# Optimization experiments

Measured on AMD Instinct MI355X. Metric: run time of the kernel, lower is better.

The kernel has to match this reference:

```python
import jax, jax.numpy as jnp
import numpy as np

B, L, S, D, H, CTX = 2, 2048, 512, 1024, 16, 1024
HD = D // H
HID = 4 * D
EPS = 1e-6


def _ln(x):
    mu = jnp.mean(x, axis=-1, keepdims=True)
    var = jnp.mean((x - mu) ** 2, axis=-1, keepdims=True)
    return (x - mu) * jax.lax.rsqrt(var + EPS)


def _rotate_half(x):
    x1, x2 = jnp.split(x, 2, axis=-1)
    return jnp.concatenate([-x2, x1], axis=-1)


def _heads(t):  # [B,N,D] -> [B,H,N,HD]
    return t.reshape(t.shape[0], t.shape[1], H, HD).transpose(0, 2, 1, 3)


def _merge(t):  # [B,H,N,HD] -> [B,N,D]
    return t.transpose(0, 2, 1, 3).reshape(t.shape[0], t.shape[2], D)


def setup_inputs() -> dict:
    key = jax.random.key(0)
    ks = jax.random.split(key, 24)
    s = 0.02
    inp = {
        "x": jax.random.normal(ks[0], (B, L, D), jnp.float32),
        "timestep_emb": jax.random.normal(ks[1], (B, D), jnp.float32),
        "context_emb": jax.random.normal(ks[2], (B, S, CTX), jnp.float32),
        "rope_emb": jax.random.normal(ks[3], (L, HD), jnp.float32),
        # adaLN modulation: Linear(D -> 6D) with bias
        "w_mod": jax.random.normal(ks[4], (D, 6 * D), jnp.float32) * s,
        "b_mod": jnp.zeros((6 * D,), jnp.float32),
        # self-attention (no qkv bias, out has bias)
        "wq_s": jax.random.normal(ks[5], (D, D), jnp.float32) * s,
        "wk_s": jax.random.normal(ks[6], (D, D), jnp.float32) * s,
        "wv_s": jax.random.normal(ks[7], (D, D), jnp.float32) * s,
        "wo_s": jax.random.normal(ks[8], (D, D), jnp.float32) * s,
        "bo_s": jnp.zeros((D,), jnp.float32),
        # cross-attention (q/k/v no bias, out has bias)
        "wq_c": jax.random.normal(ks[9], (D, D), jnp.float32) * s,
        "wk_c": jax.random.normal(ks[10], (CTX, D), jnp.float32) * s,
        "wv_c": jax.random.normal(ks[11], (CTX, D), jnp.float32) * s,
        "wo_c": jax.random.normal(ks[12], (D, D), jnp.float32) * s,
        "bo_c": jnp.zeros((D,), jnp.float32),
        # MLP
        "w1": jax.random.normal(ks[13], (D, HID), jnp.float32) * s,
        "b1": jnp.zeros((HID,), jnp.float32),
        "w2": jax.random.normal(ks[14], (HID, D), jnp.float32) * s,
        "b2": jnp.zeros((D,), jnp.float32),
    }
    return inp


def reference(x, timestep_emb, context_emb, rope_emb,
              w_mod, b_mod,
              wq_s, wk_s, wv_s, wo_s, bo_s,
              wq_c, wk_c, wv_c, wo_c, bo_c,
              w1, b1, w2, b2):
    scale = HD ** -0.5
    # adaLN modulation from timestep embedding
    mods = jnp.split(timestep_emb @ w_mod + b_mod, 6, axis=-1)
    shift_msa, scale_msa, gate_msa, shift_mlp, scale_mlp, gate_mlp = mods

    # --- self-attention with RoPE ---
    nx = _ln(x) * (1.0 + scale_msa[:, None, :]) + shift_msa[:, None, :]
    q = _heads(nx @ wq_s)
    k = _heads(nx @ wk_s)
    v = _heads(nx @ wv_s)
    cos = jnp.cos(rope_emb)[None, None]  # [1,1,L,HD]
    sin = jnp.sin(rope_emb)[None, None]
    q = q * cos + _rotate_half(q) * sin
    k = k * cos + _rotate_half(k) * sin
    attn = jax.nn.softmax(jnp.einsum("bhqd,bhkd->bhqk", q, k) * scale, axis=-1)
    sa = _merge(jnp.einsum("bhqk,bhkd->bhqd", attn, v)) @ wo_s + bo_s
    x = x + gate_msa[:, None, :] * sa

    # --- cross-attention (no mask) ---
    nx = _ln(x)
    q = _heads(nx @ wq_c)
    k = _heads(context_emb @ wk_c)
    v = _heads(context_emb @ wv_c)
    attn = jax.nn.softmax(jnp.einsum("bhqd,bhkd->bhqk", q, k) * scale, axis=-1)
    ca = _merge(jnp.einsum("bhqk,bhkd->bhqd", attn, v)) @ wo_c + bo_c
    x = x + ca

    # --- MLP with modulation + gate ---
    nx = _ln(x) * (1.0 + scale_mlp[:, None, :]) + shift_mlp[:, None, :]
    h = jax.nn.gelu(nx @ w1 + b1, approximate=False)
    x = x + gate_mlp[:, None, :] * (h @ w2 + b2)
    return x
```

## Files before the change

### kernel.cpp

```cpp
#include <hip/hip_runtime.h>
#include <hip/hip_bf16.h>


typedef short short8 __attribute__((ext_vector_type(8)));
typedef float f32x4 __attribute__((ext_vector_type(4)));
typedef float f32x16 __attribute__((ext_vector_type(16)));

#define DEV __device__ __forceinline__

DEV unsigned short f2b(float f) {
  __hip_bfloat16 h = __float2bfloat16(f);
  return *reinterpret_cast<unsigned short*>(&h);
}
DEV float b2f(unsigned short u) {
  unsigned int x = ((unsigned int)u) << 16;
  return __builtin_bit_cast(float, x);
}
DEV unsigned int pk2(float lo, float hi) {
  return (unsigned int)f2b(lo) | ((unsigned int)f2b(hi) << 16);
}
DEV void vpsw(unsigned int& a, unsigned int& b) {
  asm("v_permlane32_swap_b32 %0, %1" : "+v"(a), "+v"(b));
}

#define GLB(p) ((const __attribute__((address_space(1))) void*)(p))
#define LDSP(p) ((__attribute__((address_space(3))) void*)(p))

__global__ __launch_bounds__(256) void transpose_cast(
    const float* __restrict__ in, unsigned short* __restrict__ out, int R, int C) {
  __shared__ float tile[32][33];
  int bx = blockIdx.x * 32, by = blockIdx.y * 32;
  int tx = threadIdx.x, ty = threadIdx.y;
#pragma unroll
  for (int i = ty; i < 32; i += 8)
    tile[i][tx] = in[(size_t)(by + i) * C + bx + tx];
  __syncthreads();
#pragma unroll
  for (int i = ty; i < 32; i += 8)
    out[(size_t)(bx + i) * R + by + tx] = f2b(tile[tx][i]);
}

__global__ __launch_bounds__(256) void cast_bf16(
    const float* __restrict__ in, unsigned short* __restrict__ out, int n) {
  int i = blockIdx.x * 256 + threadIdx.x;
  if (i < n) out[i] = f2b(in[i]);
}

__global__ __launch_bounds__(256) void rope_tab(
    const float* __restrict__ rope, float* __restrict__ cosT, float* __restrict__ sinT, int n) {
  int i = blockIdx.x * 256 + threadIdx.x;
  if (i < n) {
    float v = rope[i];
    cosT[i] = cosf(v);
    sinT[i] = sinf(v);
  }
}

__global__ __launch_bounds__(256) void mods_kernel(
    const float* __restrict__ te, const unsigned short* __restrict__ wmodT,
    const float* __restrict__ bmod, float* __restrict__ mods) {
  int w = blockIdx.x * 4 + (threadIdx.x >> 6);
  int lane = threadIdx.x & 63;
  int b = w / 6144, j = w % 6144;
  const unsigned short* wr = wmodT + (size_t)j * 1024;
  const float* ter = te + (size_t)b * 1024;
  int k0 = lane * 16;
  float sum = 0.f;
#pragma unroll
  for (int u = 0; u < 2; ++u) {
    short8 wv = *(const short8*)(wr + k0 + u * 8);
#pragma unroll
    for (int e = 0; e < 8; ++e)
      sum += b2f((unsigned short)wv[e]) * ter[k0 + u * 8 + e];
  }
#pragma unroll
  for (int off = 32; off >= 1; off >>= 1) sum += __shfl_down(sum, off);
  if (lane == 0) mods[(size_t)b * 6144 + j] = sum + bmod[j];
}

__global__ __launch_bounds__(256) void ln_mod(
    const float* __restrict__ x, const float* __restrict__ mods,
    unsigned short* __restrict__ out, int scale_ofs, int shift_ofs) {
  int row = blockIdx.x;
  int b = row >> 11;
  int tid = threadIdx.x;
  const float* xr = x + (size_t)row * 1024;
  float4 v = ((const float4*)xr)[tid];
  float s = v.x + v.y + v.z + v.w;
  float ss = v.x * v.x + v.y * v.y + v.z * v.z + v.w * v.w;
#pragma unroll
  for (int off = 32; off >= 1; off >>= 1) {
    s += __shfl_down(s, off);
    ss += __shfl_down(ss, off);
  }
  __shared__ float red[8];
  int wave = tid >> 6, lane = tid & 63;
  if (lane == 0) { red[wave] = s; red[4 + wave] = ss; }
  __syncthreads();
  if (tid == 0) {
    float S = red[0] + red[1] + red[2] + red[3];
    float SS = red[4] + red[5] + red[6] + red[7];
    float mu = S * (1.f / 1024.f);
    red[0] = mu;
    red[1] = SS * (1.f / 1024.f) - mu * mu;
  }
  __syncthreads();
  float mu = red[0];
  float rs = rsqrtf(red[1] + 1e-6f);
  float vv[4] = {v.x, v.y, v.z, v.w};
  unsigned short o[4];
#pragma unroll
  for (int c = 0; c < 4; ++c) {
    int col = tid * 4 + c;
    float nv = (vv[c] - mu) * rs;
    if (scale_ofs >= 0)
      nv = nv * (1.f + mods[(size_t)b * 6144 + scale_ofs + col]) +
           mods[(size_t)b * 6144 + shift_ofs + col];
    o[c] = f2b(nv);
  }
  *(ushort4*)(&out[(size_t)row * 1024 + tid * 4]) = *(const ushort4*)o;
}

__global__ __launch_bounds__(256) void rope_apply(
    unsigned short* __restrict__ qb, unsigned short* __restrict__ kb,
    const float* __restrict__ cosT, const float* __restrict__ sinT) {
  int idx = blockIdx.x * 256 + threadIdx.x;
  unsigned short* buf = blockIdx.y ? kb : qb;
  int row = idx >> 9;
  int rem = idx & 511;
  int h = rem >> 5, d = rem & 31;
  int l = row & 2047;
  size_t base = (size_t)row * 1024 + h * 64 + d;
  float x1 = b2f(buf[base]), x2 = b2f(buf[base + 32]);
  float c1 = cosT[l * 64 + d], s1 = sinT[l * 64 + d];
  float c2 = cosT[l * 64 + d + 32], s2 = sinT[l * 64 + d + 32];
  buf[base] = f2b(x1 * c1 - x2 * s1);
  buf[base + 32] = f2b(x2 * c2 + x1 * s2);
}

template <int EPI, int MI, int NJ>
DEV void gemm_epilogue(f32x4 (&acc)[MI][NJ], void* Cout, const float* bias,
                       const float* mods, int gate_ofs, const float* src,
                       int N, int rowsPerB, int m0, int n0, int wm, int wn,
                       int g, int r) {
#pragma unroll
  for (int i = 0; i < MI; ++i) {
#pragma unroll
    for (int j = 0; j < NJ; ++j) {
#pragma unroll
      for (int q = 0; q < 4; ++q) {
        size_t grow = (size_t)(m0 + wm + i * 16 + g * 4 + q);
        size_t gcol = (size_t)(n0 + wn + j * 16 + r);
        float v = acc[i][j][q];
        if constexpr (EPI == 0) {
          ((unsigned short*)Cout)[grow * N + gcol] = f2b(v);
        } else if constexpr (EPI == 1) {
          v += bias[gcol];
          float ge = 0.5f * v * (1.0f + erff(v * 0.70710678f));
          ((unsigned short*)Cout)[grow * N + gcol] = f2b(ge);
        } else if constexpr (EPI == 3) {
          size_t buf = gcol >> 10;
          ((unsigned short*)Cout)[buf * (4096ull * 1024) + grow * 1024 + (gcol & 1023)] = f2b(v);
        } else {
          v += bias[gcol];
          float gate = 1.0f;
          if (gate_ofs >= 0)
            gate = mods[(grow / rowsPerB) * 6144 + gate_ofs + gcol];
          ((float*)Cout)[grow * N + gcol] = src[grow * N + gcol] + gate * v;
        }
      }
    }
  }
}

template <int EPI>
__global__ __launch_bounds__(256, 2) void gemm_bt(
    const unsigned short* __restrict__ A, const unsigned short* __restrict__ Bt,
    void* __restrict__ Cout, const float* __restrict__ bias,
    const float* __restrict__ mods, int gate_ofs, const float* __restrict__ src,
    int M, int N, int K, int rowsPerB) {
  __shared__ unsigned short As[128 * 32];
  __shared__ unsigned short Bs[128 * 32];
  const int tid = threadIdx.x;
  const int wave = tid >> 6, lane = tid & 63;
  const int g = lane >> 4, r = lane & 15;
  const int m0 = blockIdx.y * 128, n0 = blockIdx.x * 128;
  const int wm = (wave >> 1) * 64, wn = (wave & 1) * 64;
  const int srow = lane >> 2;
  const int scol = (lane & 3) * 8;

  f32x4 acc[4][4] = {};

  for (int k0 = 0; k0 < K; k0 += 32) {
    __syncthreads();
#pragma unroll
    for (int cc = 0; cc < 4; ++cc) {
      int c = wave * 4 + cc;
      int isB = c >> 3;
      int cl = c & 7;
      int row = cl * 16 + srow;
      const unsigned short* gsrc =
          isB ? (Bt + (size_t)(n0 + row) * K + k0 + scol)
              : (A + (size_t)(m0 + row) * K + k0 + scol);
      unsigned short* ldst = (isB ? Bs : As) + cl * 512;
      __builtin_amdgcn_global_load_lds(GLB(gsrc), LDSP(ldst), 16, 0, 0);
    }
    __syncthreads();

    short8 bfr[4];
#pragma unroll
    for (int j = 0; j < 4; ++j)
      bfr[j] = *(const short8*)(&Bs[(wn + j * 16 + r) * 32 + g * 8]);
#pragma unroll
    for (int i = 0; i < 4; ++i) {
      short8 af = *(const short8*)(&As[(wm + i * 16 + r) * 32 + g * 8]);
#pragma unroll
      for (int j = 0; j < 4; ++j)
        acc[i][j] = __builtin_amdgcn_mfma_f32_16x16x32_bf16(af, bfr[j], acc[i][j], 0, 0, 0);
    }
  }
  gemm_epilogue<EPI, 4, 4>(acc, Cout, bias, mods, gate_ofs, src, N, rowsPerB,
                           m0, n0, wm, wn, g, r);
}

template <int EPI>
__global__ __launch_bounds__(256) void gemm_pipe(
    const unsigned short* __restrict__ A, const unsigned short* __restrict__ Bt,
    void* __restrict__ Cout, const float* __restrict__ bias,
    const float* __restrict__ mods, int gate_ofs, const float* __restrict__ src,
    int M, int N, int K, int rowsPerB, int mshift) {
  __shared__ unsigned short lds[4 * 16384];
  const int tid = threadIdx.x;
  const int wave = tid >> 6, lane = tid & 63;
  const int g = lane >> 4, r = lane & 15;
  const int flat = blockIdx.x;
  const int xcd = flat & 7, idx = flat >> 3;
  const int mt = xcd * (1 << mshift) + (idx & ((1 << mshift) - 1));
  const int nt = idx >> mshift;
  const int m0 = mt * 128, n0 = nt * 128;
  const int wm = (wave >> 1) * 64, wn = (wave & 1) * 64;
  const int srow8 = lane >> 3;
  const int sck = (lane & 7) ^ srow8;

  f32x4 acc[4][4] = {};

  auto stage = [&](int t, int bufi) {
    const int k0 = t * 64;
#pragma unroll
    for (int i = 0; i < 8; ++i) {
      int u = wave * 8 + i;
      int isB = u >> 4;
      int uu = u & 15;
      int rl = uu * 8 + srow8;
      const unsigned short* gsrc =
          (isB ? (Bt + (size_t)(n0 + rl) * K) : (A + (size_t)(m0 + rl) * K)) +
          k0 + sck * 8;
      unsigned short* dst = (unsigned short*)lds + bufi * 16384 + isB * 8192 + uu * 512;
      __builtin_amdgcn_global_load_lds(GLB(gsrc), LDSP(dst), 16, 0, 0);
    }
  };

  const int nt_k = K / 64;
  stage(0, 0);
  stage(1, 1);
  stage(2, 2);

  for (int t = 0; t < nt_k; ++t) {
    int rem = nt_k - t;
    if (rem >= 3) {
      asm volatile("s_waitcnt vmcnt(16)" ::: "memory");
    } else if (rem == 2) {
      asm volatile("s_waitcnt vmcnt(8)" ::: "memory");
    } else {
      asm volatile("s_waitcnt vmcnt(0)" ::: "memory");
    }
    __builtin_amdgcn_sched_barrier(0);
    __builtin_amdgcn_s_barrier();
    __builtin_amdgcn_sched_barrier(0);
    if (t + 3 < nt_k) stage(t + 3, (t + 3) & 3);

    const unsigned short* Ab = (const unsigned short*)lds + (t & 3) * 16384;
    const unsigned short* Bb = Ab + 8192;
#pragma unroll
    for (int ks = 0; ks < 2; ++ks) {
      short8 bfr[4];
#pragma unroll
      for (int j = 0; j < 4; ++j) {
        int row = wn + j * 16 + r;
        bfr[j] = *(const short8*)&Bb[row * 64 + ((g + ks * 4) ^ (r & 7)) * 8];
      }
#pragma unroll
      for (int i = 0; i < 4; ++i) {
        int row = wm + i * 16 + r;
        short8 af = *(const short8*)&Ab[row * 64 + ((g + ks * 4) ^ (r & 7)) * 8];
#pragma unroll
        for (int j = 0; j < 4; ++j)
          acc[i][j] = __builtin_amdgcn_mfma_f32_16x16x32_bf16(af, bfr[j], acc[i][j], 0, 0, 0);
      }
    }
  }
  gemm_epilogue<EPI, 4, 4>(acc, Cout, bias, mods, gate_ofs, src, N, rowsPerB,
                           m0, n0, wm, wn, g, r);
}

template <int EPI>
__global__ __launch_bounds__(256) void gemm_p2(
    const unsigned short* __restrict__ A, const unsigned short* __restrict__ Bt,
    void* __restrict__ Cout, const float* __restrict__ bias,
    const float* __restrict__ mods, int gate_ofs, const float* __restrict__ src,
    int M, int N, int K, int rowsPerB, int ntn) {
  __shared__ unsigned short lds[3 * 12288];
  const int tid = threadIdx.x;
  const int wave = tid >> 6, lane = tid & 63;
  const int g = lane >> 4, r = lane & 15;
  const int flat = blockIdx.x;
  const int nt = flat % ntn, mt = flat / ntn;
  const int m0 = mt * 64, n0 = nt * 128;
  const int wm = (wave >> 1) * 32, wn = (wave & 1) * 64;
  const int srow8 = lane >> 3;
  const int sck = (lane & 7) ^ srow8;

  f32x4 acc[2][4] = {};

  auto stage = [&](int t, int bufi) {
    const int k0 = t * 64;
    unsigned short* base = (unsigned short*)lds + bufi * 12288;
#pragma unroll
    for (int i = 0; i < 2; ++i) {
      int u = wave * 2 + i;
      int rl = u * 8 + srow8;
      const unsigned short* gsrc = A + (size_t)(m0 + rl) * K + k0 + sck * 8;
      __builtin_amdgcn_global_load_lds(GLB(gsrc), LDSP(base + u * 512), 16, 0, 0);
    }
#pragma unroll
    for (int i = 0; i < 4; ++i) {
      int u = wave * 4 + i;
      int rl = u * 8 + srow8;
      const unsigned short* gsrc = Bt + (size_t)(n0 + rl) * K + k0 + sck * 8;
      __builtin_amdgcn_global_load_lds(GLB(gsrc), LDSP(base + 4096 + u * 512), 16, 0, 0);
    }
  };

  const int ntk = K / 64;
  stage(0, 0);
  stage(1, 1);
  int cbuf = 0, sbuf = 2;

  for (int t = 0; t < ntk; ++t) {
    if (t < ntk - 1) {
      asm volatile("s_waitcnt vmcnt(6)" ::: "memory");
    } else {
      asm volatile("s_waitcnt vmcnt(0)" ::: "memory");
    }
    __builtin_amdgcn_sched_barrier(0);
    __builtin_amdgcn_s_barrier();
    __builtin_amdgcn_sched_barrier(0);
    if (t + 2 < ntk) {
      stage(t + 2, sbuf);
      sbuf = (sbuf == 2) ? 0 : sbuf + 1;
    }

    const unsigned short* Ab = (const unsigned short*)lds + cbuf * 12288;
    const unsigned short* Bb = Ab + 4096;
#pragma unroll
    for (int ks = 0; ks < 2; ++ks) {
      short8 bfr[4];
#pragma unroll
      for (int j = 0; j < 4; ++j) {
        int row = wn + j * 16 + r;
        bfr[j] = *(const short8*)&Bb[row * 64 + ((g + ks * 4) ^ (r & 7)) * 8];
      }
#pragma unroll
      for (int i = 0; i < 2; ++i) {
        int row = wm + i * 16 + r;
        short8 af = *(const short8*)&Ab[row * 64 + ((g + ks * 4) ^ (r & 7)) * 8];
#pragma unroll
        for (int j = 0; j < 4; ++j)
          acc[i][j] = __builtin_amdgcn_mfma_f32_16x16x32_bf16(af, bfr[j], acc[i][j], 0, 0, 0);
      }
    }
    cbuf = (cbuf == 2) ? 0 : cbuf + 1;
  }
  gemm_epilogue<EPI, 2, 4>(acc, Cout, bias, mods, gate_ofs, src, N, rowsPerB,
                           m0, n0, wm, wn, g, r);
}

__global__ __launch_bounds__(256, 2) void flash2(
    const unsigned short* __restrict__ Q, const unsigned short* __restrict__ Kv,
    const unsigned short* __restrict__ Vv, unsigned short* __restrict__ O,
    int Lk, float c1) {
  __shared__ unsigned short lds[16384];
  const int tid = threadIdx.x, wave = tid >> 6, lane = tid & 63;
  const int hi = lane >> 5, lq = lane & 31;
  const int flat = blockIdx.x;
  const int xcd = flat & 7, rr = flat >> 3;
  const int gl = rr >> 4, qt = rr & 15;
  const int g = xcd * 4 + gl;
  const int h = g & 15, b = g >> 4;
  const int Lq = 2048, D = 1024;

  const unsigned short* Qbase =
      Q + ((size_t)b * Lq + qt * 128 + wave * 32 + lq) * D + h * 64;
  const unsigned short* Kbase = Kv + (size_t)b * Lk * D + h * 64;
  const unsigned short* Vbase = Vv + (size_t)b * Lk * D + h * 64;

  short8 qf[4];
#pragma unroll
  for (int kb = 0; kb < 4; ++kb)
    qf[kb] = *(const short8*)(Qbase + kb * 16 + hi * 8);

  const short8 ones = {0x3F80, 0x3F80, 0x3F80, 0x3F80, 0x3F80, 0x3F80, 0x3F80, 0x3F80};

  const int kr0 = tid >> 3, kc0 = tid & 7;
  const int kvp = tid >> 3, db = tid & 7;
  const int kch0 = (kc0 ^ (kr0 & 7) ^ (kr0 >> 3)) & 7;
  const int kch1 = kch0 ^ 4;
  const int f0 = (lq & 7) ^ (lq >> 3);
  const int swz0 = f0 << 4, swz1 = swz0 ^ 64;

  int vby[8];
#pragma unroll
  for (int e = 0; e < 8; ++e) {
    int d = db * 8 + e;
    vby[e] = d * 128 + ((kvp * 4) ^ (((e ^ db) & 7) << 4));
  }

  float m_run = -3.0e38f;
  f32x16 o0 = {}, o1 = {}, lacc = {};
  short8 vr0, vr1;

  {
    const unsigned short* v0 = Vbase + (size_t)(2 * kvp) * D + db * 8;
    vr0 = *(const short8*)v0;
    vr1 = *(const short8*)(v0 + D);
    const unsigned short* s0 = Kbase + (size_t)kr0 * D + kch0 * 8;
    const unsigned short* s1 = Kbase + (size_t)(kr0 + 32) * D + kch1 * 8;
    __builtin_amdgcn_global_load_lds(GLB(s0), LDSP(&lds[wave * 512]), 16, 0, 0);
    __builtin_amdgcn_global_load_lds(GLB(s1), LDSP(&lds[2048 + wave * 512]), 16, 0, 0);
    char* vt = (char*)&lds[8192];
#pragma unroll
    for (int e = 0; e < 8; ++e)
      *(unsigned int*)(vt + vby[e]) =
          (unsigned int)(unsigned short)vr0[e] |
          ((unsigned int)(unsigned short)vr1[e] << 16);
  }
  __syncthreads();

  const int nkt = Lk / 64;
  int cb = 0;
  for (int kt = 0; kt < nkt; ++kt) {
    const bool pf = (kt + 1 < nkt);
    if (pf) {
      const unsigned short* v0 = Vbase + (size_t)((kt + 1) * 64 + 2 * kvp) * D + db * 8;
      vr0 = *(const short8*)v0;
      vr1 = *(const short8*)(v0 + D);
      const int nb = (cb ^ 1) * 4096;
      const unsigned short* s0 = Kbase + (size_t)((kt + 1) * 64 + kr0) * D + kch0 * 8;
      const unsigned short* s1 = Kbase + (size_t)((kt + 1) * 64 + kr0 + 32) * D + kch1 * 8;
      __builtin_amdgcn_global_load_lds(GLB(s0), LDSP(&lds[nb + wave * 512]), 16, 0, 0);
      __builtin_amdgcn_global_load_lds(GLB(s1), LDSP(&lds[nb + 2048 + wave * 512]), 16, 0, 0);
    }

    f32x16 s0a = {}, s1a = {};
    {
      const unsigned short* K0 = &lds[cb * 4096];
#pragma unroll
      for (int ks = 0; ks < 4; ++ks) {
        int lo = ks * 32 + hi * 16;
        short8 a0 = *(const short8*)&K0[lq * 64 + ((lo ^ swz0) >> 1)];
        short8 a1 = *(const short8*)&K0[(32 + lq) * 64 + ((lo ^ swz1) >> 1)];
        s0a = __builtin_amdgcn_mfma_f32_32x32x16_bf16(a0, qf[ks], s0a, 0, 0, 0);
        s1a = __builtin_amdgcn_mfma_f32_32x32x16_bf16(a1, qf[ks], s1a, 0, 0, 0);
      }
    }

    float tm[8];
#pragma unroll
    for (int i = 0; i < 8; ++i)
      tm[i] = fmaxf(fmaxf(s0a[i], s0a[i + 8]), fmaxf(s1a[i], s1a[i + 8]));
    float pm = fmaxf(fmaxf(fmaxf(tm[0], tm[1]), fmaxf(tm[2], tm[3])),
                     fmaxf(fmaxf(tm[4], tm[5]), fmaxf(tm[6], tm[7])));
    {
      unsigned int ua = __builtin_bit_cast(unsigned int, pm), ub = ua;
      vpsw(ua, ub);
      pm = fmaxf(__builtin_bit_cast(float, ua), __builtin_bit_cast(float, ub));
    }
    if (__any((pm - m_run) * c1 > 8.0f)) {
      float mnew = fmaxf(m_run, pm);
      float alpha = exp2f((m_run - mnew) * c1);
      lacc[0] *= alpha;
#pragma unroll
      for (int i = 0; i < 16; ++i) { o0[i] *= alpha; o1[i] *= alpha; }
      m_run = mnew;
    }
    float mc = m_run * c1;
#pragma unroll
    for (int i = 0; i < 16; ++i) s0a[i] = exp2f(s0a[i] * c1 - mc);
#pragma unroll
    for (int i = 0; i < 16; ++i) s1a[i] = exp2f(s1a[i] * c1 - mc);

    short8 pbf[4];
#pragma unroll
    for (int kb = 0; kb < 4; ++kb) {
      int bb = (kb & 1) * 8;
      float p0, p1, p2, p3, p4, p5, p6, p7;
      if (kb < 2) {
        p0 = s0a[bb + 0]; p1 = s0a[bb + 1]; p2 = s0a[bb + 2]; p3 = s0a[bb + 3];
        p4 = s0a[bb + 4]; p5 = s0a[bb + 5]; p6 = s0a[bb + 6]; p7 = s0a[bb + 7];
      } else {
        p0 = s1a[bb + 0]; p1 = s1a[bb + 1]; p2 = s1a[bb + 2]; p3 = s1a[bb + 3];
        p4 = s1a[bb + 4]; p5 = s1a[bb + 5]; p6 = s1a[bb + 6]; p7 = s1a[bb + 7];
      }
      unsigned int u0 = pk2(p0, p1), u1 = pk2(p2, p3);
      unsigned int u2 = pk2(p4, p5), u3 = pk2(p6, p7);
      vpsw(u0, u2);
      vpsw(u1, u3);
      union { unsigned int u[4]; short8 s; } fr;
      fr.u[0] = u0; fr.u[1] = u1; fr.u[2] = u2; fr.u[3] = u3;
      pbf[kb] = fr.s;
    }

    if (pf) {
      char* vt = (char*)&lds[8192 + (cb ^ 1) * 4096];
#pragma unroll
      for (int e = 0; e < 8; ++e)
        *(unsigned int*)(vt + vby[e]) =
            (unsigned int)(unsigned short)vr0[e] |
            ((unsigned int)(unsigned short)vr1[e] << 16);
    }

    {
      const unsigned short* V0 = &lds[8192 + cb * 4096];
#pragma unroll
      for (int kb = 0; kb < 4; ++kb) {
        int lo = kb * 32 + hi * 16;
        short8 vf0 = *(const short8*)&V0[lq * 64 + ((lo ^ swz0) >> 1)];
        short8 vf1 = *(const short8*)&V0[(32 + lq) * 64 + ((lo ^ swz1) >> 1)];
        o0 = __builtin_amdgcn_mfma_f32_32x32x16_bf16(vf0, pbf[kb], o0, 0, 0, 0);
        o1 = __builtin_amdgcn_mfma_f32_32x32x16_bf16(vf1, pbf[kb], o1, 0, 0, 0);
        lacc = __builtin_amdgcn_mfma_f32_32x32x16_bf16(ones, pbf[kb], lacc, 0, 0, 0);
      }
    }

    __syncthreads();
    cb ^= 1;
  }

  __syncthreads();
  float rl = 1.0f / lacc[0];
  unsigned short* os = &lds[wave * 2048];
#pragma unroll
  for (int t = 0; t < 2; ++t) {
#pragma unroll
    for (int c = 0; c < 4; ++c) {
      int dbase = 32 * t + 8 * c + 4 * hi;
      float v0 = (t ? o1[4 * c + 0] : o0[4 * c + 0]) * rl;
      float v1 = (t ? o1[4 * c + 1] : o0[4 * c + 1]) * rl;
      float v2 = (t ? o1[4 * c + 2] : o0[4 * c + 2]) * rl;
      float v3 = (t ? o1[4 * c + 3] : o0[4 * c + 3]) * rl;
      int by0 = lq * 128 + ((dbase * 2) ^ ((lq & 7) << 4));
      int by1 = lq * 128 + (((dbase + 2) * 2) ^ ((lq & 7) << 4));
      *(unsigned int*)((char*)os + by0) = pk2(v0, v1);
      *(unsigned int*)((char*)os + by1) = pk2(v2, v3);
    }
  }
  int q2 = lane >> 1;
  unsigned short* orow =
      O + ((size_t)b * Lq + qt * 128 + wave * 32 + q2) * D + h * 64;
#pragma unroll
  for (int j = 0; j < 4; ++j) {
    int j2 = (lane & 1) * 4 + j;
    int byr = q2 * 128 + ((j2 * 16) ^ ((q2 & 7) << 4));
    short8 vv = *(const short8*)((char*)os + byr);
    *(short8*)(orow + j2 * 8) = vv;
  }
}

extern "C" void kernel_launch(void* const* d_in, const int* in_sizes, int n_in,
                              void* d_out, int out_size, void* d_ws, size_t ws_size,
                              hipStream_t stream) {
  (void)in_sizes; (void)n_in; (void)out_size; (void)ws_size;
  const float* x_in = (const float*)d_in[0];
  const float* te   = (const float*)d_in[1];
  const float* ctx  = (const float*)d_in[2];
  const float* rope = (const float*)d_in[3];
  const float* wmod = (const float*)d_in[4];
  const float* bmod = (const float*)d_in[5];
  const float* wqs  = (const float*)d_in[6];
  const float* wks  = (const float*)d_in[7];
  const float* wvs  = (const float*)d_in[8];
  const float* wos  = (const float*)d_in[9];
  const float* bos  = (const float*)d_in[10];
  const float* wqc  = (const float*)d_in[11];
  const float* wkc  = (const float*)d_in[12];
  const float* wvc  = (const float*)d_in[13];
  const float* woc  = (const float*)d_in[14];
  const float* boc  = (const float*)d_in[15];
  const float* w1   = (const float*)d_in[16];
  const float* b1   = (const float*)d_in[17];
  const float* w2   = (const float*)d_in[18];
  const float* b2   = (const float*)d_in[19];
  float* out = (float*)d_out;

  char* w = (char*)d_ws;
  size_t o = 0;
  auto alloc = [&](size_t bytes) {
    char* p = w + o;
    o = (o + bytes + 255) & ~(size_t)255;
    return p;
  };
  unsigned short* wmodT = (unsigned short*)alloc(6144ull * 1024 * 2);
  unsigned short* wqsT  = (unsigned short*)alloc(1024ull * 1024 * 2);
  unsigned short* wksT  = (unsigned short*)alloc(1024ull * 1024 * 2);
  unsigned short* wvsT  = (unsigned short*)alloc(1024ull * 1024 * 2);
  unsigned short* wosT  = (unsigned short*)alloc(1024ull * 1024 * 2);
  unsigned short* wqcT  = (unsigned short*)alloc(1024ull * 1024 * 2);
  unsigned short* wkcT  = (unsigned short*)alloc(1024ull * 1024 * 2);
  unsigned short* wvcT  = (unsigned short*)alloc(1024ull * 1024 * 2);
  unsigned short* wocT  = (unsigned short*)alloc(1024ull * 1024 * 2);
  unsigned short* w1T   = (unsigned short*)alloc(4096ull * 1024 * 2);
  unsigned short* w2T   = (unsigned short*)alloc(1024ull * 4096 * 2);
  float* modsb = (float*)alloc(2ull * 6144 * 4);
  float* cosT  = (float*)alloc(2048ull * 64 * 4);
  float* sinT  = (float*)alloc(2048ull * 64 * 4);
  unsigned short* nx   = (unsigned short*)alloc(4096ull * 1024 * 2);
  unsigned short* ctxb = (unsigned short*)alloc(1024ull * 1024 * 2);
  unsigned short* qb = (unsigned short*)alloc(4096ull * 1024 * 2);
  unsigned short* kb = (unsigned short*)alloc(4096ull * 1024 * 2);
  unsigned short* vb = (unsigned short*)alloc(4096ull * 1024 * 2);
  unsigned short* ao = (unsigned short*)alloc(4096ull * 1024 * 2);
  float* xw = (float*)alloc(4096ull * 1024 * 4);
  unsigned short* hbuf = qb;

  const float c1 = 0.125f * 1.4426950408889634f;

  dim3 tb(32, 8);
  transpose_cast<<<dim3(6144 / 32, 1024 / 32), tb, 0, stream>>>(wmod, wmodT, 1024, 6144);
  transpose_cast<<<dim3(32, 32), tb, 0, stream>>>(wqs, wqsT, 1024, 1024);
  transpose_cast<<<dim3(32, 32), tb, 0, stream>>>(wks, wksT, 1024, 1024);
  transpose_cast<<<dim3(32, 32), tb, 0, stream>>>(wvs, wvsT, 1024, 1024);
  transpose_cast<<<dim3(32, 32), tb, 0, stream>>>(wos, wosT, 1024, 1024);
  transpose_cast<<<dim3(32, 32), tb, 0, stream>>>(wqc, wqcT, 1024, 1024);
  transpose_cast<<<dim3(32, 32), tb, 0, stream>>>(wkc, wkcT, 1024, 1024);
  transpose_cast<<<dim3(32, 32), tb, 0, stream>>>(wvc, wvcT, 1024, 1024);
  transpose_cast<<<dim3(32, 32), tb, 0, stream>>>(woc, wocT, 1024, 1024);
  transpose_cast<<<dim3(4096 / 32, 1024 / 32), tb, 0, stream>>>(w1, w1T, 1024, 4096);
  transpose_cast<<<dim3(1024 / 32, 4096 / 32), tb, 0, stream>>>(w2, w2T, 4096, 1024);

  cast_bf16<<<4096, 256, 0, stream>>>(ctx, ctxb, 1024 * 1024);
  rope_tab<<<512, 256, 0, stream>>>(rope, cosT, sinT, 2048 * 64);
  mods_kernel<<<3072, 256, 0, stream>>>(te, wmodT, bmod, modsb);

  ln_mod<<<4096, 256, 0, stream>>>(x_in, modsb, nx, 1024, 0);
  gemm_pipe<3><<<768, 256, 0, stream>>>(nx, wqsT, qb, nullptr, nullptr, -1, nullptr, 4096, 3072, 1024, 2048, 2);
  rope_apply<<<dim3(8192, 2), 256, 0, stream>>>(qb, kb, cosT, sinT);
  flash2<<<512, 256, 0, stream>>>(qb, kb, vb, ao, 2048, c1);
  gemm_p2<2><<<512, 256, 0, stream>>>(ao, wosT, xw, bos, modsb, 2048, x_in, 4096, 1024, 1024, 2048, 8);

  ln_mod<<<4096, 256, 0, stream>>>(xw, modsb, nx, -1, -1);
  gemm_p2<0><<<512, 256, 0, stream>>>(nx, wqcT, qb, nullptr, nullptr, -1, nullptr, 4096, 1024, 1024, 2048, 8);
  gemm_p2<3><<<256, 256, 0, stream>>>(ctxb, wkcT, kb, nullptr, nullptr, -1, nullptr, 1024, 2048, 1024, 512, 16);
  flash2<<<512, 256, 0, stream>>>(qb, kb, vb, ao, 512, c1);
  gemm_p2<2><<<512, 256, 0, stream>>>(ao, wocT, xw, boc, modsb, -1, xw, 4096, 1024, 1024, 2048, 8);

  ln_mod<<<4096, 256, 0, stream>>>(xw, modsb, nx, 4096, 3072);
  gemm_bt<1><<<dim3(32, 32), 256, 0, stream>>>(nx, w1T, hbuf, b1, nullptr, -1, nullptr, 4096, 4096, 1024, 2048);
  gemm_p2<2><<<512, 256, 0, stream>>>(hbuf, w2T, out, b2, modsb, 5120, xw, 4096, 1024, 4096, 2048, 8);
}
```

Measured before the change: 425.7 us.

## Split KV tile across wave pairs in flash attention and merge partial softmax

Rewrites the flash attention kernel so each block covers 64 query rows instead of 128. The four waves form two pairs, each pair handling one 32-key half of every 64-key tile, and the partial max, row sum and output of the two halves are merged through LDS at the end. The grid doubles to 1024 blocks and the launch bound asks for 4 blocks per CU, which is meant to raise occupancy and shorten per-wave dependency chains. In exchange, each K/V tile now feeds half as many query rows, so global K/V traffic per query doubles. It also adds an end-of-kernel reduction pass and a new V LDS layout.

```diff
diff --git a/kernel.cpp b/kernel.cpp
--- a/kernel.cpp
+++ b/kernel.cpp
@@ -385,22 +385,23 @@
                            m0, n0, wm, wn, g, r);
 }
 
-__global__ __launch_bounds__(256, 2) void flash2(
+__global__ __launch_bounds__(256, 4) void flash3(
     const unsigned short* __restrict__ Q, const unsigned short* __restrict__ Kv,
     const unsigned short* __restrict__ Vv, unsigned short* __restrict__ O,
     int Lk, float c1) {
   __shared__ unsigned short lds[16384];
   const int tid = threadIdx.x, wave = tid >> 6, lane = tid & 63;
   const int hi = lane >> 5, lq = lane & 31;
+  const int qh = wave & 1, p = wave >> 1;
   const int flat = blockIdx.x;
   const int xcd = flat & 7, rr = flat >> 3;
-  const int gl = rr >> 4, qt = rr & 15;
+  const int gl = rr >> 5, qt = rr & 31;
   const int g = xcd * 4 + gl;
   const int h = g & 15, b = g >> 4;
   const int Lq = 2048, D = 1024;
 
   const unsigned short* Qbase =
-      Q + ((size_t)b * Lq + qt * 128 + wave * 32 + lq) * D + h * 64;
+      Q + ((size_t)b * Lq + qt * 64 + qh * 32 + lq) * D + h * 64;
   const unsigned short* Kbase = Kv + (size_t)b * Lk * D + h * 64;
   const unsigned short* Vbase = Vv + (size_t)b * Lk * D + h * 64;
 
@@ -412,18 +413,21 @@
   const short8 ones = {0x3F80, 0x3F80, 0x3F80, 0x3F80, 0x3F80, 0x3F80, 0x3F80, 0x3F80};
 
   const int kr0 = tid >> 3, kc0 = tid & 7;
+  const int kch0 = (kc0 ^ (kr0 & 7) ^ (kr0 >> 3)) & 7;
   const int kvp = tid >> 3, db = tid & 7;
-  const int kch0 = (kc0 ^ (kr0 & 7) ^ (kr0 >> 3)) & 7;
-  const int kch1 = kch0 ^ 4;
-  const int f0 = (lq & 7) ^ (lq >> 3);
-  const int swz0 = f0 << 4, swz1 = swz0 ^ 64;
+  const int vpar = kvp >> 4;
+  const int kvl = kvp & 15;
 
   int vby[8];
 #pragma unroll
   for (int e = 0; e < 8; ++e) {
     int d = db * 8 + e;
-    vby[e] = d * 128 + ((kvp * 4) ^ (((e ^ db) & 7) << 4));
-  }
+    vby[e] = d * 64 + ((kvl * 4) ^ ((((e ^ db)) & 3) << 4));
+  }
+
+  const int f0 = (lq & 7) ^ (lq >> 3);
+  const int swz0 = f0 << 4;
+  const int vsw = (f0 & 3) << 4;
 
   float m_run = -3.0e38f;
   f32x16 o0 = {}, o1 = {}, lacc = {};
@@ -434,10 +438,10 @@
     vr0 = *(const short8*)v0;
     vr1 = *(const short8*)(v0 + D);
     const unsigned short* s0 = Kbase + (size_t)kr0 * D + kch0 * 8;
-    const unsigned short* s1 = Kbase + (size_t)(kr0 + 32) * D + kch1 * 8;
+    const unsigned short* s1 = Kbase + (size_t)(kr0 + 32) * D + kch0 * 8;
     __builtin_amdgcn_global_load_lds(GLB(s0), LDSP(&lds[wave * 512]), 16, 0, 0);
     __builtin_amdgcn_global_load_lds(GLB(s1), LDSP(&lds[2048 + wave * 512]), 16, 0, 0);
-    char* vt = (char*)&lds[8192];
+    char* vt = (char*)lds + 16384 + vpar * 4096;
 #pragma unroll
     for (int e = 0; e < 8; ++e)
       *(unsigned int*)(vt + vby[e]) =
@@ -446,40 +450,36 @@
   }
   __syncthreads();
 
-  const int nkt = Lk / 64;
+  const int nit = Lk / 64;
   int cb = 0;
-  for (int kt = 0; kt < nkt; ++kt) {
-    const bool pf = (kt + 1 < nkt);
+  for (int it = 0; it < nit; ++it) {
+    const bool pf = (it + 1 < nit);
     if (pf) {
-      const unsigned short* v0 = Vbase + (size_t)((kt + 1) * 64 + 2 * kvp) * D + db * 8;
+      const unsigned short* v0 = Vbase + (size_t)((it + 1) * 64 + 2 * kvp) * D + db * 8;
       vr0 = *(const short8*)v0;
       vr1 = *(const short8*)(v0 + D);
-      const int nb = (cb ^ 1) * 4096;
-      const unsigned short* s0 = Kbase + (size_t)((kt + 1) * 64 + kr0) * D + kch0 * 8;
-      const unsigned short* s1 = Kbase + (size_t)((kt + 1) * 64 + kr0 + 32) * D + kch1 * 8;
-      __builtin_amdgcn_global_load_lds(GLB(s0), LDSP(&lds[nb + wave * 512]), 16, 0, 0);
-      __builtin_amdgcn_global_load_lds(GLB(s1), LDSP(&lds[nb + 2048 + wave * 512]), 16, 0, 0);
-    }
-
-    f32x16 s0a = {}, s1a = {};
+      const int nb = cb ^ 1;
+      const unsigned short* s0 = Kbase + (size_t)((it + 1) * 64 + kr0) * D + kch0 * 8;
+      const unsigned short* s1 = Kbase + (size_t)((it + 1) * 64 + kr0 + 32) * D + kch0 * 8;
+      __builtin_amdgcn_global_load_lds(GLB(s0), LDSP(&lds[nb * 4096 + wave * 512]), 16, 0, 0);
+      __builtin_amdgcn_global_load_lds(GLB(s1), LDSP(&lds[nb * 4096 + 2048 + wave * 512]), 16, 0, 0);
+    }
+
+    f32x16 sa = {};
     {
-      const unsigned short* K0 = &lds[cb * 4096];
+      const unsigned short* K0 = &lds[cb * 4096 + p * 2048];
 #pragma unroll
       for (int ks = 0; ks < 4; ++ks) {
         int lo = ks * 32 + hi * 16;
         short8 a0 = *(const short8*)&K0[lq * 64 + ((lo ^ swz0) >> 1)];
-        short8 a1 = *(const short8*)&K0[(32 + lq) * 64 + ((lo ^ swz1) >> 1)];
-        s0a = __builtin_amdgcn_mfma_f32_32x32x16_bf16(a0, qf[ks], s0a, 0, 0, 0);
-        s1a = __builtin_amdgcn_mfma_f32_32x32x16_bf16(a1, qf[ks], s1a, 0, 0, 0);
-      }
-    }
-
-    float tm[8];
-#pragma unroll
-    for (int i = 0; i < 8; ++i)
-      tm[i] = fmaxf(fmaxf(s0a[i], s0a[i + 8]), fmaxf(s1a[i], s1a[i + 8]));
-    float pm = fmaxf(fmaxf(fmaxf(tm[0], tm[1]), fmaxf(tm[2], tm[3])),
-                     fmaxf(fmaxf(tm[4], tm[5]), fmaxf(tm[6], tm[7])));
+        sa = __builtin_amdgcn_mfma_f32_32x32x16_bf16(a0, qf[ks], sa, 0, 0, 0);
+      }
+    }
+
+    float pm = fmaxf(fmaxf(fmaxf(sa[0], sa[1]), fmaxf(sa[2], sa[3])),
+                     fmaxf(fmaxf(sa[4], sa[5]), fmaxf(sa[6], sa[7])));
+    pm = fmaxf(pm, fmaxf(fmaxf(fmaxf(sa[8], sa[9]), fmaxf(sa[10], sa[11])),
+                         fmaxf(fmaxf(sa[12], sa[13]), fmaxf(sa[14], sa[15]))));
     {
       unsigned int ua = __builtin_bit_cast(unsigned int, pm), ub = ua;
       vpsw(ua, ub);
@@ -495,24 +495,14 @@
     }
     float mc = m_run * c1;
 #pragma unroll
-    for (int i = 0; i < 16; ++i) s0a[i] = exp2f(s0a[i] * c1 - mc);
-#pragma unroll
-    for (int i = 0; i < 16; ++i) s1a[i] = exp2f(s1a[i] * c1 - mc);
-
-    short8 pbf[4];
-#pragma unroll
-    for (int kb = 0; kb < 4; ++kb) {
-      int bb = (kb & 1) * 8;
-      float p0, p1, p2, p3, p4, p5, p6, p7;
-      if (kb < 2) {
-        p0 = s0a[bb + 0]; p1 = s0a[bb + 1]; p2 = s0a[bb + 2]; p3 = s0a[bb + 3];
-        p4 = s0a[bb + 4]; p5 = s0a[bb + 5]; p6 = s0a[bb + 6]; p7 = s0a[bb + 7];
-      } else {
-        p0 = s1a[bb + 0]; p1 = s1a[bb + 1]; p2 = s1a[bb + 2]; p3 = s1a[bb + 3];
-        p4 = s1a[bb + 4]; p5 = s1a[bb + 5]; p6 = s1a[bb + 6]; p7 = s1a[bb + 7];
-      }
-      unsigned int u0 = pk2(p0, p1), u1 = pk2(p2, p3);
-      unsigned int u2 = pk2(p4, p5), u3 = pk2(p6, p7);
+    for (int i = 0; i < 16; ++i) sa[i] = exp2f(sa[i] * c1 - mc);
+
+    short8 pbf[2];
+#pragma unroll
+    for (int kb = 0; kb < 2; ++kb) {
+      int bb = kb * 8;
+      unsigned int u0 = pk2(sa[bb + 0], sa[bb + 1]), u1 = pk2(sa[bb + 2], sa[bb + 3]);
+      unsigned int u2 = pk2(sa[bb + 4], sa[bb + 5]), u3 = pk2(sa[bb + 6], sa[bb + 7]);
       vpsw(u0, u2);
       vpsw(u1, u3);
       union { unsigned int u[4]; short8 s; } fr;
@@ -521,7 +511,7 @@
     }
 
     if (pf) {
-      char* vt = (char*)&lds[8192 + (cb ^ 1) * 4096];
+      char* vt = (char*)lds + 16384 + (cb ^ 1) * 8192 + vpar * 4096;
 #pragma unroll
       for (int e = 0; e < 8; ++e)
         *(unsigned int*)(vt + vby[e]) =
@@ -530,12 +520,12 @@
     }
 
     {
-      const unsigned short* V0 = &lds[8192 + cb * 4096];
-#pragma unroll
-      for (int kb = 0; kb < 4; ++kb) {
+      const unsigned short* V0 = &lds[8192 + cb * 4096 + p * 2048];
+#pragma unroll
+      for (int kb = 0; kb < 2; ++kb) {
         int lo = kb * 32 + hi * 16;
-        short8 vf0 = *(const short8*)&V0[lq * 64 + ((lo ^ swz0) >> 1)];
-        short8 vf1 = *(const short8*)&V0[(32 + lq) * 64 + ((lo ^ swz1) >> 1)];
+        short8 vf0 = *(const short8*)&V0[lq * 32 + ((lo ^ vsw) >> 1)];
+        short8 vf1 = *(const short8*)&V0[(lq + 32) * 32 + ((lo ^ vsw) >> 1)];
         o0 = __builtin_amdgcn_mfma_f32_32x32x16_bf16(vf0, pbf[kb], o0, 0, 0, 0);
         o1 = __builtin_amdgcn_mfma_f32_32x32x16_bf16(vf1, pbf[kb], o1, 0, 0, 0);
         lacc = __builtin_amdgcn_mfma_f32_32x32x16_bf16(ones, pbf[kb], lacc, 0, 0, 0);
@@ -546,33 +536,59 @@
     cb ^= 1;
   }
 
+  const float m_own = m_run, l_own = lacc[0];
+  float* ex = (float*)lds;
+  if (p == 1) {
+    ex[qh * 64 + lane] = m_own;
+    ex[128 + qh * 64 + lane] = l_own;
+    float* ob = ex + 256 + qh * 2048;
+#pragma unroll
+    for (int t = 0; t < 16; ++t) {
+      ob[t * 64 + lane] = o0[t];
+      ob[(16 + t) * 64 + lane] = o1[t];
+    }
+  }
   __syncthreads();
-  float rl = 1.0f / lacc[0];
-  unsigned short* os = &lds[wave * 2048];
-#pragma unroll
-  for (int t = 0; t < 2; ++t) {
-#pragma unroll
-    for (int c = 0; c < 4; ++c) {
-      int dbase = 32 * t + 8 * c + 4 * hi;
-      float v0 = (t ? o1[4 * c + 0] : o0[4 * c + 0]) * rl;
-      float v1 = (t ? o1[4 * c + 1] : o0[4 * c + 1]) * rl;
-      float v2 = (t ? o1[4 * c + 2] : o0[4 * c + 2]) * rl;
-      float v3 = (t ? o1[4 * c + 3] : o0[4 * c + 3]) * rl;
-      int by0 = lq * 128 + ((dbase * 2) ^ ((lq & 7) << 4));
-      int by1 = lq * 128 + (((dbase + 2) * 2) ^ ((lq & 7) << 4));
-      *(unsigned int*)((char*)os + by0) = pk2(v0, v1);
-      *(unsigned int*)((char*)os + by1) = pk2(v2, v3);
-    }
-  }
-  int q2 = lane >> 1;
-  unsigned short* orow =
-      O + ((size_t)b * Lq + qt * 128 + wave * 32 + q2) * D + h * 64;
-#pragma unroll
-  for (int j = 0; j < 4; ++j) {
-    int j2 = (lane & 1) * 4 + j;
-    int byr = q2 * 128 + ((j2 * 16) ^ ((q2 & 7) << 4));
-    short8 vv = *(const short8*)((char*)os + byr);
-    *(short8*)(orow + j2 * 8) = vv;
+  if (p == 0) {
+    float m1v = ex[qh * 64 + lane];
+    float l1v = ex[128 + qh * 64 + lane];
+    float mM = fmaxf(m_own, m1v);
+    float a0s = exp2f((m_own - mM) * c1);
+    float a1s = exp2f((m1v - mM) * c1);
+    float rl = 1.0f / (a0s * l_own + a1s * l1v);
+    const float* ob = ex + 256 + qh * 2048;
+#pragma unroll
+    for (int t = 0; t < 16; ++t) {
+      o0[t] = (a0s * o0[t] + a1s * ob[t * 64 + lane]) * rl;
+      o1[t] = (a0s * o1[t] + a1s * ob[(16 + t) * 64 + lane]) * rl;
+    }
+
+    unsigned short* os = (unsigned short*)lds + 8704 + qh * 2048;
+#pragma unroll
+    for (int t = 0; t < 2; ++t) {
+#pragma unroll
+      for (int c = 0; c < 4; ++c) {
+        int dbase = 32 * t + 8 * c + 4 * hi;
+        float v0 = (t ? o1[4 * c + 0] : o0[4 * c + 0]);
+        float v1 = (t ? o1[4 * c + 1] : o0[4 * c + 1]);
+        float v2 = (t ? o1[4 * c + 2] : o0[4 * c + 2]);
+        float v3 = (t ? o1[4 * c + 3] : o0[4 * c + 3]);
+        int by0 = lq * 128 + ((dbase * 2) ^ ((lq & 7) << 4));
+        int by1 = lq * 128 + (((dbase + 2) * 2) ^ ((lq & 7) << 4));
+        *(unsigned int*)((char*)os + by0) = pk2(v0, v1);
+        *(unsigned int*)((char*)os + by1) = pk2(v2, v3);
+      }
+    }
+    int q2 = lane >> 1;
+    unsigned short* orow =
+        O + ((size_t)b * Lq + qt * 64 + qh * 32 + q2) * D + h * 64;
+#pragma unroll
+    for (int j = 0; j < 4; ++j) {
+      int j2 = (lane & 1) * 4 + j;
+      int byr = q2 * 128 + ((j2 * 16) ^ ((q2 & 7) << 4));
+      short8 vv = *(const short8*)((char*)os + byr);
+      *(short8*)(orow + j2 * 8) = vv;
+    }
   }
 }
 
@@ -654,13 +670,13 @@
   ln_mod<<<4096, 256, 0, stream>>>(x_in, modsb, nx, 1024, 0);
   gemm_pipe<3><<<768, 256, 0, stream>>>(nx, wqsT, qb, nullptr, nullptr, -1, nullptr, 4096, 3072, 1024, 2048, 2);
   rope_apply<<<dim3(8192, 2), 256, 0, stream>>>(qb, kb, cosT, sinT);
-  flash2<<<512, 256, 0, stream>>>(qb, kb, vb, ao, 2048, c1);
+  flash3<<<1024, 256, 0, stream>>>(qb, kb, vb, ao, 2048, c1);
   gemm_p2<2><<<512, 256, 0, stream>>>(ao, wosT, xw, bos, modsb, 2048, x_in, 4096, 1024, 1024, 2048, 8);
 
   ln_mod<<<4096, 256, 0, stream>>>(xw, modsb, nx, -1, -1);
   gemm_p2<0><<<512, 256, 0, stream>>>(nx, wqcT, qb, nullptr, nullptr, -1, nullptr, 4096, 1024, 1024, 2048, 8);
   gemm_p2<3><<<256, 256, 0, stream>>>(ctxb, wkcT, kb, nullptr, nullptr, -1, nullptr, 1024, 2048, 1024, 512, 16);
-  flash2<<<512, 256, 0, stream>>>(qb, kb, vb, ao, 512, c1);
+  flash3<<<1024, 256, 0, stream>>>(qb, kb, vb, ao, 512, c1);
   gemm_p2<2><<<512, 256, 0, stream>>>(ao, wocT, xw, boc, modsb, -1, xw, 4096, 1024, 1024, 2048, 8);
 
   ln_mod<<<4096, 256, 0, stream>>>(xw, modsb, nx, 4096, 3072);
```

New measurement: 437.5 us. +2.8%, slower.
